# Optimization experiments

Measured on AMD Instinct MI355X. Metric: run time of the kernel, lower is better.

Reference implementation:

```python
import jax, jax.numpy as jnp
import numpy as np

DIM = 256
WINDOW = 8
NUM_HEADS = 8
N = WINDOW * WINDOW  # tokens per window
HEAD_DIM = DIM // NUM_HEADS
SCALE = HEAD_DIM ** -0.5
B_ = 2048


def _relative_position_index(w):
    coords = np.stack(np.meshgrid(np.arange(w), np.arange(w), indexing='ij'))  # 2,w,w
    cf = coords.reshape(2, -1)  # 2,N
    rel = cf[:, :, None] - cf[:, None, :]  # 2,N,N
    rel = rel.transpose(1, 2, 0) + (w - 1)  # N,N,2 in [0, 2w-2]
    return rel[..., 0] * (2 * w - 1) + rel[..., 1]  # N,N

REL_INDEX = jnp.asarray(_relative_position_index(WINDOW))  # (N,N) int


def setup_inputs() -> dict:
    key = jax.random.key(0)
    ks = jax.random.split(key, 8)
    x = jax.random.normal(ks[0], (B_, N, DIM), dtype=jnp.float32)
    mask = jax.random.normal(ks[1], (B_, 1, N, N), dtype=jnp.float32)
    w_qkv = jax.random.normal(ks[2], (3 * DIM, DIM), dtype=jnp.float32) * (DIM ** -0.5)
    b_qkv = jnp.zeros((3 * DIM,), dtype=jnp.float32)
    w_proj = jax.random.normal(ks[3], (DIM, DIM), dtype=jnp.float32) * (DIM ** -0.5)
    b_proj = jnp.zeros((DIM,), dtype=jnp.float32)
    bias_table = jax.random.normal(ks[4], ((2 * WINDOW - 1) ** 2, NUM_HEADS), dtype=jnp.float32) * 0.02
    return {"x": x, "mask": mask, "w_qkv": w_qkv, "b_qkv": b_qkv,
            "w_proj": w_proj, "b_proj": b_proj, "bias_table": bias_table}


def reference(x, mask, w_qkv, b_qkv, w_proj, b_proj, bias_table):
    Bw, n, c = x.shape
    qkv = x @ w_qkv.T + b_qkv  # (B_, N, 3*C)
    qkv = qkv.reshape(Bw, n, 3, NUM_HEADS, HEAD_DIM)
    q = qkv[:, :, 0].transpose(0, 2, 1, 3) * SCALE  # (B_, H, N, hd)
    k = qkv[:, :, 1].transpose(0, 2, 1, 3)
    v = qkv[:, :, 2].transpose(0, 2, 1, 3)
    attn = jnp.einsum('bhnd,bhmd->bhnm', q, k)  # (B_, H, N, N)
    rel_bias = bias_table[REL_INDEX]  # (N, N, H)
    attn = attn + rel_bias.transpose(2, 0, 1)[None]  # broadcast (1,H,N,N)
    attn = attn + mask  # (B_,1,N,N) broadcasts over heads
    attn = jax.nn.softmax(attn, axis=-1)
    out = jnp.einsum('bhnm,bhmd->bhnd', attn, v)  # (B_, H, N, hd)
    out = out.transpose(0, 2, 1, 3).reshape(Bw, n, c)
    return out @ w_proj.T + b_proj
```

## Files before the change

### kernel.cpp

```cpp
#include <hip/hip_runtime.h>

#define NWIN 2048
#define NTOK 64
#define CDIM 256
#define NH 8
#define HD 32
#define QSCALE 0.17677669529663689f

#define LDA 264

typedef __bf16 bf16x8 __attribute__((ext_vector_type(8)));
typedef float  f32x4  __attribute__((ext_vector_type(4)));
typedef unsigned int u32x4 __attribute__((ext_vector_type(4)));

__device__ __forceinline__ unsigned short f2bf(float f) {
    union { float f; unsigned u; } v; v.f = f;
    unsigned r = v.u + 0x7FFFu + ((v.u >> 16) & 1u);
    return (unsigned short)(r >> 16);
}

__device__ __forceinline__ bf16x8 ld16(const unsigned short* p) {
    return *(const bf16x8*)p;
}

__device__ __forceinline__ unsigned cvtpk(float lo, float hi) {
    unsigned r;
    asm("v_cvt_pk_bf16_f32 %0, %1, %2" : "=v"(r) : "v"(lo), "v"(hi));
    return r;
}
__device__ __forceinline__ void pl32(unsigned &a, unsigned &b) {
    asm("v_permlane32_swap_b32 %0, %1" : "+v"(a), "+v"(b));
}
__device__ __forceinline__ void pl16(unsigned &a, unsigned &b) {
    asm("v_permlane16_swap_b32 %0, %1" : "+v"(a), "+v"(b));
}

__device__ __forceinline__ bf16x8 xchg32(f32x4 t0, f32x4 t1) {
    unsigned u00 = cvtpk(t0[0], t0[1]);
    unsigned u01 = cvtpk(t0[2], t0[3]);
    unsigned u10 = cvtpk(t1[0], t1[1]);
    unsigned u11 = cvtpk(t1[2], t1[3]);
    pl32(u00, u10);
    pl32(u01, u11);
    pl16(u00, u10);
    pl16(u01, u11);
    union { u32x4 u; bf16x8 v; } r;
    r.u = (u32x4){u00, u01, u10, u11};
    return r.v;
}

__global__ void precast_kernel(const float* __restrict__ wq, const float* __restrict__ wp,
                               const float* __restrict__ bt,
                               unsigned short* __restrict__ wqb, unsigned short* __restrict__ wpb,
                               float* __restrict__ relbQ) {
    int i = blockIdx.x * 256 + threadIdx.x;
    if (i < 196608) {
        wqb[i] = f2bf(wq[i]);
    } else if (i < 262144) {
        wpb[i - 196608] = f2bf(wp[i - 196608]);
    } else if (i < 294912) {
        int j = i - 262144;
        int h = j >> 12;
        int q = (j >> 6) & 63;
        int k = j & 63;
        int yq = q >> 3, xq = q & 7, yk = k >> 3, xk = k & 7;
        int idx = (yq - yk + 7) * 15 + (xq - xk + 7);
        relbQ[j] = bt[idx * NH + h];
    }
}

__global__ __launch_bounds__(512, 4)
void win_attn_kernel(const float* __restrict__ x, const float* __restrict__ mask,
                     const float* __restrict__ bq, const float* __restrict__ bp,
                     const unsigned short* __restrict__ wq, const unsigned short* __restrict__ wp,
                     const float* __restrict__ relbQ, float* __restrict__ out) {
    __shared__ __align__(16) unsigned short sm[NTOK * LDA + NH * 4 * 64 * 8];
    unsigned short* sX = sm;
    unsigned short* sK = sm + NTOK * LDA;

    const int b    = blockIdx.x;
    const int tid  = threadIdx.x;
    const int wv   = tid >> 6;
    const int lane = tid & 63;
    const int lm   = lane & 15;
    const int quad = lane >> 4;
    const f32x4 fzero = {0.f, 0.f, 0.f, 0.f};

    {
        const int row = tid >> 3;
        const int c0  = (tid & 7) * 32;
        const float4* gx = (const float4*)(x + ((size_t)b * NTOK + row) * CDIM + c0);
        unsigned short* dst = sX + row * LDA + c0;
        #pragma unroll
        for (int i = 0; i < 4; ++i) {
            float4 a = gx[2 * i];
            float4 c = gx[2 * i + 1];
            u32x4 w = { cvtpk(a.x, a.y), cvtpk(a.z, a.w), cvtpk(c.x, c.y), cvtpk(c.z, c.w) };
            *(u32x4*)(dst + i * 8) = w;
        }
    }
    __syncthreads();

    const int h = wv;

    {
        f32x4 a0[4], a1[4];
        #pragma unroll
        for (int nt = 0; nt < 4; ++nt) { a0[nt] = fzero; a1[nt] = fzero; }
        const unsigned short* w0 = wq + (CDIM + h*HD + lm) * CDIM;
        const unsigned short* w1 = wq + (CDIM + h*HD + 16 + lm) * CDIM;
        #pragma unroll
        for (int ks = 0; ks < 8; ++ks) {
            bf16x8 xa[4];
            #pragma unroll
            for (int nt = 0; nt < 4; ++nt)
                xa[nt] = ld16(sX + (nt * 16 + lm) * LDA + ks * 32 + quad * 8);
            bf16x8 wf0 = ld16(w0 + ks * 32 + quad * 8);
            bf16x8 wf1 = ld16(w1 + ks * 32 + quad * 8);
            #pragma unroll
            for (int nt = 0; nt < 4; ++nt) {
                a0[nt] = __builtin_amdgcn_mfma_f32_16x16x32_bf16(wf0, xa[nt], a0[nt], 0, 0, 0);
                a1[nt] = __builtin_amdgcn_mfma_f32_16x16x32_bf16(wf1, xa[nt], a1[nt], 0, 0, 0);
            }
        }
        const float4 b0 = *(const float4*)(bq + CDIM + h*HD + quad*4);
        const float4 b1 = *(const float4*)(bq + CDIM + h*HD + 16 + quad*4);
        const float b0v[4] = {b0.x, b0.y, b0.z, b0.w};
        const float b1v[4] = {b1.x, b1.y, b1.z, b1.w};
        #pragma unroll
        for (int nt = 0; nt < 4; ++nt) {
            #pragma unroll
            for (int r = 0; r < 4; ++r) { a0[nt][r] += b0v[r]; a1[nt][r] += b1v[r]; }
            bf16x8 kfrag = xchg32(a0[nt], a1[nt]);
            *(bf16x8*)(sK + ((h * 4 + nt) * 64 + lane) * 8) = kfrag;
        }
    }

    bf16x8 qf[4];
    {
        f32x4 a0[4], a1[4];
        #pragma unroll
        for (int nt = 0; nt < 4; ++nt) { a0[nt] = fzero; a1[nt] = fzero; }
        const unsigned short* w0 = wq + (h*HD + lm) * CDIM;
        const unsigned short* w1 = wq + (h*HD + 16 + lm) * CDIM;
        #pragma unroll
        for (int ks = 0; ks < 8; ++ks) {
            bf16x8 xa[4];
            #pragma unroll
            for (int nt = 0; nt < 4; ++nt)
                xa[nt] = ld16(sX + (nt * 16 + lm) * LDA + ks * 32 + quad * 8);
            bf16x8 wf0 = ld16(w0 + ks * 32 + quad * 8);
            bf16x8 wf1 = ld16(w1 + ks * 32 + quad * 8);
            #pragma unroll
            for (int nt = 0; nt < 4; ++nt) {
                a0[nt] = __builtin_amdgcn_mfma_f32_16x16x32_bf16(wf0, xa[nt], a0[nt], 0, 0, 0);
                a1[nt] = __builtin_amdgcn_mfma_f32_16x16x32_bf16(wf1, xa[nt], a1[nt], 0, 0, 0);
            }
        }
        const float4 b0 = *(const float4*)(bq + h*HD + quad*4);
        const float4 b1 = *(const float4*)(bq + h*HD + 16 + quad*4);
        const float b0v[4] = {b0.x, b0.y, b0.z, b0.w};
        const float b1v[4] = {b1.x, b1.y, b1.z, b1.w};
        #pragma unroll
        for (int nt = 0; nt < 4; ++nt) {
            #pragma unroll
            for (int r = 0; r < 4; ++r) {
                a0[nt][r] = (a0[nt][r] + b0v[r]) * QSCALE;
                a1[nt][r] = (a1[nt][r] + b1v[r]) * QSCALE;
            }
            qf[nt] = xchg32(a0[nt], a1[nt]);
        }
    }

    bf16x8 vf[2][2];
    #pragma unroll
    for (int t = 0; t < 2; ++t) {
        f32x4 va[4];
        #pragma unroll
        for (int mt = 0; mt < 4; ++mt) va[mt] = fzero;
        const unsigned short* wvp = wq + (2*CDIM + h*HD + t*16 + lm) * CDIM;
        #pragma unroll
        for (int ks = 0; ks < 8; ++ks) {
            bf16x8 xa[4];
            #pragma unroll
            for (int mt = 0; mt < 4; ++mt)
                xa[mt] = ld16(sX + (mt * 16 + lm) * LDA + ks * 32 + quad * 8);
            bf16x8 wfv = ld16(wvp + ks * 32 + quad * 8);
            #pragma unroll
            for (int mt = 0; mt < 4; ++mt)
                va[mt] = __builtin_amdgcn_mfma_f32_16x16x32_bf16(xa[mt], wfv, va[mt], 0, 0, 0);
        }
        const float bV = bq[2*CDIM + h*HD + t*16 + lm];
        #pragma unroll
        for (int mt = 0; mt < 4; ++mt)
            #pragma unroll
            for (int r = 0; r < 4; ++r) va[mt][r] += bV;
        vf[t][0] = xchg32(va[0], va[1]);
        vf[t][1] = xchg32(va[2], va[3]);
    }
    __syncthreads();

    {
        const float* maskb = mask + (size_t)b * (NTOK * NTOK);
        const float* relh  = relbQ + h * (NTOK * NTOK);
        const unsigned short* sKh = sK + h * 4 * 64 * 8;

        #pragma unroll
        for (int rc = 0; rc < 4; ++rc) {
            f32x4 s[4];
            #pragma unroll
            for (int jt = 0; jt < 4; ++jt) {
                bf16x8 kf = ld16(sKh + (jt * 64 + lane) * 8);
                s[jt] = __builtin_amdgcn_mfma_f32_16x16x32_bf16(kf, qf[rc], fzero, 0, 0, 0);
            }

            const float* mrow = maskb + (rc * 16 + lm) * 64;
            const float* rrow = relh  + (rc * 16 + lm) * 64;
            #pragma unroll
            for (int jt = 0; jt < 4; ++jt) {
                float4 rb = *(const float4*)(rrow + jt * 16 + quad * 4);
                float4 mk = *(const float4*)(mrow + jt * 16 + quad * 4);
                const float rbv[4] = {rb.x, rb.y, rb.z, rb.w};
                const float mkv[4] = {mk.x, mk.y, mk.z, mk.w};
                #pragma unroll
                for (int r = 0; r < 4; ++r) s[jt][r] += rbv[r] + mkv[r];
            }

            float mx = s[0][0];
            #pragma unroll
            for (int jt = 0; jt < 4; ++jt)
                #pragma unroll
                for (int r = 0; r < 4; ++r) mx = fmaxf(mx, s[jt][r]);
            mx = fmaxf(mx, __shfl_xor(mx, 16, 64));
            mx = fmaxf(mx, __shfl_xor(mx, 32, 64));

            float sum = 0.f;
            #pragma unroll
            for (int jt = 0; jt < 4; ++jt)
                #pragma unroll
                for (int r = 0; r < 4; ++r) {
                    float e = __expf(s[jt][r] - mx);
                    s[jt][r] = e;
                    sum += e;
                }
            sum += __shfl_xor(sum, 16, 64);
            sum += __shfl_xor(sum, 32, 64);
            const float inv = 1.0f / sum;

            bf16x8 pb0 = xchg32(s[0], s[1]);
            bf16x8 pb1 = xchg32(s[2], s[3]);

            f32x4 o0 = __builtin_amdgcn_mfma_f32_16x16x32_bf16(vf[0][0], pb0, fzero, 0, 0, 0);
            o0 = __builtin_amdgcn_mfma_f32_16x16x32_bf16(vf[0][1], pb1, o0, 0, 0, 0);
            f32x4 o1 = __builtin_amdgcn_mfma_f32_16x16x32_bf16(vf[1][0], pb0, fzero, 0, 0, 0);
            o1 = __builtin_amdgcn_mfma_f32_16x16x32_bf16(vf[1][1], pb1, o1, 0, 0, 0);
            #pragma unroll
            for (int r = 0; r < 4; ++r) { o0[r] *= inv; o1[r] *= inv; }

            bf16x8 ob = xchg32(o0, o1);
            *(bf16x8*)(sX + (rc * 16 + lm) * LDA + h * HD + quad * 8) = ob;
        }
    }
    __syncthreads();

    {
        const int n0 = wv * HD;
        f32x4 acc[4][2];
        #pragma unroll
        for (int mt = 0; mt < 4; ++mt) { acc[mt][0] = fzero; acc[mt][1] = fzero; }

        #pragma unroll
        for (int ks = 0; ks < 8; ++ks) {
            bf16x8 bfr[2];
            #pragma unroll
            for (int nt = 0; nt < 2; ++nt)
                bfr[nt] = ld16(wp + (n0 + nt * 16 + lm) * CDIM + ks * 32 + quad * 8);
            bf16x8 afr[4];
            #pragma unroll
            for (int mt = 0; mt < 4; ++mt)
                afr[mt] = ld16(sX + (mt * 16 + lm) * LDA + ks * 32 + quad * 8);
            #pragma unroll
            for (int mt = 0; mt < 4; ++mt)
                #pragma unroll
                for (int nt = 0; nt < 2; ++nt)
                    acc[mt][nt] = __builtin_amdgcn_mfma_f32_16x16x32_bf16(afr[mt], bfr[nt], acc[mt][nt], 0, 0, 0);
        }

        float bpv[2] = { bp[n0 + lm], bp[n0 + 16 + lm] };
        #pragma unroll
        for (int mt = 0; mt < 4; ++mt)
            #pragma unroll
            for (int nt = 0; nt < 2; ++nt)
                #pragma unroll
                for (int reg = 0; reg < 4; ++reg) {
                    int r = mt * 16 + quad * 4 + reg;
                    out[((size_t)b * NTOK + r) * CDIM + n0 + nt * 16 + lm] = acc[mt][nt][reg] + bpv[nt];
                }
    }
}

extern "C" void kernel_launch(void* const* d_in, const int* in_sizes, int n_in,
                              void* d_out, int out_size, void* d_ws, size_t ws_size,
                              hipStream_t stream) {
    const float* x    = (const float*)d_in[0];
    const float* mask = (const float*)d_in[1];
    const float* wq   = (const float*)d_in[2];
    const float* bq   = (const float*)d_in[3];
    const float* wp   = (const float*)d_in[4];
    const float* bp   = (const float*)d_in[5];
    const float* bt   = (const float*)d_in[6];

    unsigned short* wqb   = (unsigned short*)d_ws;
    unsigned short* wpb   = wqb + 196608;
    float*          relbQ = (float*)((char*)d_ws + 524288);
    float*          out   = (float*)d_out;

    precast_kernel<<<1152, 256, 0, stream>>>(wq, wp, bt, wqb, wpb, relbQ);
    win_attn_kernel<<<NWIN, 512, 0, stream>>>(x, mask, bq, bp, wqb, wpb, relbQ, out);
}
```

Baseline: 461.1 us.

## Process two windows per block to reuse rel-bias loads and halve grid

Each 512-thread block now handles two windows instead of one. It stages both inputs in a doubled shared-memory buffer, holds Q and V fragments for both windows in registers, and loads the relative-position bias once per row chunk for both windows. The V projection is also reworked to load both weight halves in a single k-loop. The aim is to amortise weight and bias fetches and per-block overhead across two windows. The cost is higher register and LDS use, which lowers occupancy (launch bounds drop from 4 to 2 blocks per CU) and halves the grid to 1024 blocks.

```diff
diff --git a/kernel.cpp b/kernel.cpp
--- a/kernel.cpp
+++ b/kernel.cpp
@@ -8,6 +8,7 @@
 #define QSCALE 0.17677669529663689f
 
 #define LDA 264
+#define SKW (NH * 4 * 64 * 8)
 
 typedef __bf16 bf16x8 __attribute__((ext_vector_type(8)));
 typedef float  f32x4  __attribute__((ext_vector_type(4)));
@@ -69,16 +70,14 @@
     }
 }
 
-__global__ __launch_bounds__(512, 4)
+__global__ __launch_bounds__(512, 2)
 void win_attn_kernel(const float* __restrict__ x, const float* __restrict__ mask,
                      const float* __restrict__ bq, const float* __restrict__ bp,
                      const unsigned short* __restrict__ wq, const unsigned short* __restrict__ wp,
                      const float* __restrict__ relbQ, float* __restrict__ out) {
-    __shared__ __align__(16) unsigned short sm[NTOK * LDA + NH * 4 * 64 * 8];
-    unsigned short* sX = sm;
-    unsigned short* sK = sm + NTOK * LDA;
-
-    const int b    = blockIdx.x;
+    __shared__ __align__(16) unsigned short sm[2 * NTOK * LDA + 2 * SKW];
+
+    const int b0   = blockIdx.x * 2;
     const int tid  = threadIdx.x;
     const int wv   = tid >> 6;
     const int lane = tid & 63;
@@ -89,213 +88,244 @@
     {
         const int row = tid >> 3;
         const int c0  = (tid & 7) * 32;
-        const float4* gx = (const float4*)(x + ((size_t)b * NTOK + row) * CDIM + c0);
-        unsigned short* dst = sX + row * LDA + c0;
         #pragma unroll
-        for (int i = 0; i < 4; ++i) {
-            float4 a = gx[2 * i];
-            float4 c = gx[2 * i + 1];
-            u32x4 w = { cvtpk(a.x, a.y), cvtpk(a.z, a.w), cvtpk(c.x, c.y), cvtpk(c.z, c.w) };
-            *(u32x4*)(dst + i * 8) = w;
+        for (int w = 0; w < 2; ++w) {
+            const float4* gx = (const float4*)(x + ((size_t)(b0 + w) * NTOK + row) * CDIM + c0);
+            unsigned short* dst = sm + w * (NTOK * LDA) + row * LDA + c0;
+            #pragma unroll
+            for (int i = 0; i < 4; ++i) {
+                float4 a = gx[2 * i];
+                float4 c = gx[2 * i + 1];
+                u32x4 v = { cvtpk(a.x, a.y), cvtpk(a.z, a.w), cvtpk(c.x, c.y), cvtpk(c.z, c.w) };
+                *(u32x4*)(dst + i * 8) = v;
+            }
         }
     }
     __syncthreads();
 
     const int h = wv;
 
+    bf16x8 qf[2][4];
+    bf16x8 vf[2][2][2];
+    #pragma unroll
+    for (int w = 0; w < 2; ++w) {
+        const unsigned short* sXw = sm + w * (NTOK * LDA);
+        unsigned short* sKw = sm + 2 * (NTOK * LDA) + w * SKW;
+
+        {
+            f32x4 a0[4], a1[4];
+            #pragma unroll
+            for (int nt = 0; nt < 4; ++nt) { a0[nt] = fzero; a1[nt] = fzero; }
+            const unsigned short* w0 = wq + (CDIM + h*HD + lm) * CDIM;
+            const unsigned short* w1 = wq + (CDIM + h*HD + 16 + lm) * CDIM;
+            #pragma unroll
+            for (int ks = 0; ks < 8; ++ks) {
+                bf16x8 xa[4];
+                #pragma unroll
+                for (int nt = 0; nt < 4; ++nt)
+                    xa[nt] = ld16(sXw + (nt * 16 + lm) * LDA + ks * 32 + quad * 8);
+                bf16x8 wf0 = ld16(w0 + ks * 32 + quad * 8);
+                bf16x8 wf1 = ld16(w1 + ks * 32 + quad * 8);
+                #pragma unroll
+                for (int nt = 0; nt < 4; ++nt) {
+                    a0[nt] = __builtin_amdgcn_mfma_f32_16x16x32_bf16(wf0, xa[nt], a0[nt], 0, 0, 0);
+                    a1[nt] = __builtin_amdgcn_mfma_f32_16x16x32_bf16(wf1, xa[nt], a1[nt], 0, 0, 0);
+                }
+            }
+            const float4 bk0 = *(const float4*)(bq + CDIM + h*HD + quad*4);
+            const float4 bk1 = *(const float4*)(bq + CDIM + h*HD + 16 + quad*4);
+            const float b0v[4] = {bk0.x, bk0.y, bk0.z, bk0.w};
+            const float b1v[4] = {bk1.x, bk1.y, bk1.z, bk1.w};
+            #pragma unroll
+            for (int nt = 0; nt < 4; ++nt) {
+                #pragma unroll
+                for (int r = 0; r < 4; ++r) { a0[nt][r] += b0v[r]; a1[nt][r] += b1v[r]; }
+                bf16x8 kfrag = xchg32(a0[nt], a1[nt]);
+                *(bf16x8*)(sKw + ((h * 4 + nt) * 64 + lane) * 8) = kfrag;
+            }
+        }
+
+        {
+            f32x4 a0[4], a1[4];
+            #pragma unroll
+            for (int nt = 0; nt < 4; ++nt) { a0[nt] = fzero; a1[nt] = fzero; }
+            const unsigned short* w0 = wq + (h*HD + lm) * CDIM;
+            const unsigned short* w1 = wq + (h*HD + 16 + lm) * CDIM;
+            #pragma unroll
+            for (int ks = 0; ks < 8; ++ks) {
+                bf16x8 xa[4];
+                #pragma unroll
+                for (int nt = 0; nt < 4; ++nt)
+                    xa[nt] = ld16(sXw + (nt * 16 + lm) * LDA + ks * 32 + quad * 8);
+                bf16x8 wf0 = ld16(w0 + ks * 32 + quad * 8);
+                bf16x8 wf1 = ld16(w1 + ks * 32 + quad * 8);
+                #pragma unroll
+                for (int nt = 0; nt < 4; ++nt) {
+                    a0[nt] = __builtin_amdgcn_mfma_f32_16x16x32_bf16(wf0, xa[nt], a0[nt], 0, 0, 0);
+                    a1[nt] = __builtin_amdgcn_mfma_f32_16x16x32_bf16(wf1, xa[nt], a1[nt], 0, 0, 0);
+                }
+            }
+            const float4 bq0 = *(const float4*)(bq + h*HD + quad*4);
+            const float4 bq1 = *(const float4*)(bq + h*HD + 16 + quad*4);
+            const float b0v[4] = {bq0.x, bq0.y, bq0.z, bq0.w};
+            const float b1v[4] = {bq1.x, bq1.y, bq1.z, bq1.w};
+            #pragma unroll
+            for (int nt = 0; nt < 4; ++nt) {
+                #pragma unroll
+                for (int r = 0; r < 4; ++r) {
+                    a0[nt][r] = (a0[nt][r] + b0v[r]) * QSCALE;
+                    a1[nt][r] = (a1[nt][r] + b1v[r]) * QSCALE;
+                }
+                qf[w][nt] = xchg32(a0[nt], a1[nt]);
+            }
+        }
+
+        {
+            f32x4 va[4][2];
+            #pragma unroll
+            for (int mt = 0; mt < 4; ++mt) { va[mt][0] = fzero; va[mt][1] = fzero; }
+            #pragma unroll
+            for (int ks = 0; ks < 8; ++ks) {
+                bf16x8 xa[4], wfv[2];
+                #pragma unroll
+                for (int mt = 0; mt < 4; ++mt)
+                    xa[mt] = ld16(sXw + (mt * 16 + lm) * LDA + ks * 32 + quad * 8);
+                #pragma unroll
+                for (int t = 0; t < 2; ++t)
+                    wfv[t] = ld16(wq + (2*CDIM + h*HD + t*16 + lm) * CDIM + ks * 32 + quad * 8);
+                #pragma unroll
+                for (int mt = 0; mt < 4; ++mt)
+                    #pragma unroll
+                    for (int t = 0; t < 2; ++t)
+                        va[mt][t] = __builtin_amdgcn_mfma_f32_16x16x32_bf16(xa[mt], wfv[t], va[mt][t], 0, 0, 0);
+            }
+            const float bV0 = bq[2*CDIM + h*HD + lm];
+            const float bV1 = bq[2*CDIM + h*HD + 16 + lm];
+            #pragma unroll
+            for (int mt = 0; mt < 4; ++mt)
+                #pragma unroll
+                for (int r = 0; r < 4; ++r) { va[mt][0][r] += bV0; va[mt][1][r] += bV1; }
+            #pragma unroll
+            for (int t = 0; t < 2; ++t) {
+                vf[w][t][0] = xchg32(va[0][t], va[1][t]);
+                vf[w][t][1] = xchg32(va[2][t], va[3][t]);
+            }
+        }
+    }
+    __syncthreads();
+
     {
-        f32x4 a0[4], a1[4];
-        #pragma unroll
-        for (int nt = 0; nt < 4; ++nt) { a0[nt] = fzero; a1[nt] = fzero; }
-        const unsigned short* w0 = wq + (CDIM + h*HD + lm) * CDIM;
-        const unsigned short* w1 = wq + (CDIM + h*HD + 16 + lm) * CDIM;
-        #pragma unroll
-        for (int ks = 0; ks < 8; ++ks) {
-            bf16x8 xa[4];
-            #pragma unroll
-            for (int nt = 0; nt < 4; ++nt)
-                xa[nt] = ld16(sX + (nt * 16 + lm) * LDA + ks * 32 + quad * 8);
-            bf16x8 wf0 = ld16(w0 + ks * 32 + quad * 8);
-            bf16x8 wf1 = ld16(w1 + ks * 32 + quad * 8);
-            #pragma unroll
-            for (int nt = 0; nt < 4; ++nt) {
-                a0[nt] = __builtin_amdgcn_mfma_f32_16x16x32_bf16(wf0, xa[nt], a0[nt], 0, 0, 0);
-                a1[nt] = __builtin_amdgcn_mfma_f32_16x16x32_bf16(wf1, xa[nt], a1[nt], 0, 0, 0);
-            }
-        }
-        const float4 b0 = *(const float4*)(bq + CDIM + h*HD + quad*4);
-        const float4 b1 = *(const float4*)(bq + CDIM + h*HD + 16 + quad*4);
-        const float b0v[4] = {b0.x, b0.y, b0.z, b0.w};
-        const float b1v[4] = {b1.x, b1.y, b1.z, b1.w};
-        #pragma unroll
-        for (int nt = 0; nt < 4; ++nt) {
-            #pragma unroll
-            for (int r = 0; r < 4; ++r) { a0[nt][r] += b0v[r]; a1[nt][r] += b1v[r]; }
-            bf16x8 kfrag = xchg32(a0[nt], a1[nt]);
-            *(bf16x8*)(sK + ((h * 4 + nt) * 64 + lane) * 8) = kfrag;
-        }
-    }
-
-    bf16x8 qf[4];
-    {
-        f32x4 a0[4], a1[4];
-        #pragma unroll
-        for (int nt = 0; nt < 4; ++nt) { a0[nt] = fzero; a1[nt] = fzero; }
-        const unsigned short* w0 = wq + (h*HD + lm) * CDIM;
-        const unsigned short* w1 = wq + (h*HD + 16 + lm) * CDIM;
-        #pragma unroll
-        for (int ks = 0; ks < 8; ++ks) {
-            bf16x8 xa[4];
-            #pragma unroll
-            for (int nt = 0; nt < 4; ++nt)
-                xa[nt] = ld16(sX + (nt * 16 + lm) * LDA + ks * 32 + quad * 8);
-            bf16x8 wf0 = ld16(w0 + ks * 32 + quad * 8);
-            bf16x8 wf1 = ld16(w1 + ks * 32 + quad * 8);
-            #pragma unroll
-            for (int nt = 0; nt < 4; ++nt) {
-                a0[nt] = __builtin_amdgcn_mfma_f32_16x16x32_bf16(wf0, xa[nt], a0[nt], 0, 0, 0);
-                a1[nt] = __builtin_amdgcn_mfma_f32_16x16x32_bf16(wf1, xa[nt], a1[nt], 0, 0, 0);
-            }
-        }
-        const float4 b0 = *(const float4*)(bq + h*HD + quad*4);
-        const float4 b1 = *(const float4*)(bq + h*HD + 16 + quad*4);
-        const float b0v[4] = {b0.x, b0.y, b0.z, b0.w};
-        const float b1v[4] = {b1.x, b1.y, b1.z, b1.w};
-        #pragma unroll
-        for (int nt = 0; nt < 4; ++nt) {
-            #pragma unroll
-            for (int r = 0; r < 4; ++r) {
-                a0[nt][r] = (a0[nt][r] + b0v[r]) * QSCALE;
-                a1[nt][r] = (a1[nt][r] + b1v[r]) * QSCALE;
-            }
-            qf[nt] = xchg32(a0[nt], a1[nt]);
-        }
-    }
-
-    bf16x8 vf[2][2];
-    #pragma unroll
-    for (int t = 0; t < 2; ++t) {
-        f32x4 va[4];
-        #pragma unroll
-        for (int mt = 0; mt < 4; ++mt) va[mt] = fzero;
-        const unsigned short* wvp = wq + (2*CDIM + h*HD + t*16 + lm) * CDIM;
-        #pragma unroll
-        for (int ks = 0; ks < 8; ++ks) {
-            bf16x8 xa[4];
-            #pragma unroll
-            for (int mt = 0; mt < 4; ++mt)
-                xa[mt] = ld16(sX + (mt * 16 + lm) * LDA + ks * 32 + quad * 8);
-            bf16x8 wfv = ld16(wvp + ks * 32 + quad * 8);
-            #pragma unroll
-            for (int mt = 0; mt < 4; ++mt)
-                va[mt] = __builtin_amdgcn_mfma_f32_16x16x32_bf16(xa[mt], wfv, va[mt], 0, 0, 0);
-        }
-        const float bV = bq[2*CDIM + h*HD + t*16 + lm];
-        #pragma unroll
-        for (int mt = 0; mt < 4; ++mt)
-            #pragma unroll
-            for (int r = 0; r < 4; ++r) va[mt][r] += bV;
-        vf[t][0] = xchg32(va[0], va[1]);
-        vf[t][1] = xchg32(va[2], va[3]);
-    }
-    __syncthreads();
-
-    {
-        const float* maskb = mask + (size_t)b * (NTOK * NTOK);
-        const float* relh  = relbQ + h * (NTOK * NTOK);
-        const unsigned short* sKh = sK + h * 4 * 64 * 8;
+        const float* relh = relbQ + h * (NTOK * NTOK);
 
         #pragma unroll
         for (int rc = 0; rc < 4; ++rc) {
-            f32x4 s[4];
-            #pragma unroll
-            for (int jt = 0; jt < 4; ++jt) {
-                bf16x8 kf = ld16(sKh + (jt * 64 + lane) * 8);
-                s[jt] = __builtin_amdgcn_mfma_f32_16x16x32_bf16(kf, qf[rc], fzero, 0, 0, 0);
-            }
-
-            const float* mrow = maskb + (rc * 16 + lm) * 64;
-            const float* rrow = relh  + (rc * 16 + lm) * 64;
-            #pragma unroll
-            for (int jt = 0; jt < 4; ++jt) {
-                float4 rb = *(const float4*)(rrow + jt * 16 + quad * 4);
-                float4 mk = *(const float4*)(mrow + jt * 16 + quad * 4);
-                const float rbv[4] = {rb.x, rb.y, rb.z, rb.w};
-                const float mkv[4] = {mk.x, mk.y, mk.z, mk.w};
-                #pragma unroll
-                for (int r = 0; r < 4; ++r) s[jt][r] += rbv[r] + mkv[r];
-            }
-
-            float mx = s[0][0];
+            const float* rrow = relh + (rc * 16 + lm) * 64;
+            float4 rb[4];
             #pragma unroll
             for (int jt = 0; jt < 4; ++jt)
-                #pragma unroll
-                for (int r = 0; r < 4; ++r) mx = fmaxf(mx, s[jt][r]);
-            mx = fmaxf(mx, __shfl_xor(mx, 16, 64));
-            mx = fmaxf(mx, __shfl_xor(mx, 32, 64));
-
-            float sum = 0.f;
-            #pragma unroll
-            for (int jt = 0; jt < 4; ++jt)
-                #pragma unroll
-                for (int r = 0; r < 4; ++r) {
-                    float e = __expf(s[jt][r] - mx);
-                    s[jt][r] = e;
-                    sum += e;
-                }
-            sum += __shfl_xor(sum, 16, 64);
-            sum += __shfl_xor(sum, 32, 64);
-            const float inv = 1.0f / sum;
-
-            bf16x8 pb0 = xchg32(s[0], s[1]);
-            bf16x8 pb1 = xchg32(s[2], s[3]);
-
-            f32x4 o0 = __builtin_amdgcn_mfma_f32_16x16x32_bf16(vf[0][0], pb0, fzero, 0, 0, 0);
-            o0 = __builtin_amdgcn_mfma_f32_16x16x32_bf16(vf[0][1], pb1, o0, 0, 0, 0);
-            f32x4 o1 = __builtin_amdgcn_mfma_f32_16x16x32_bf16(vf[1][0], pb0, fzero, 0, 0, 0);
-            o1 = __builtin_amdgcn_mfma_f32_16x16x32_bf16(vf[1][1], pb1, o1, 0, 0, 0);
-            #pragma unroll
-            for (int r = 0; r < 4; ++r) { o0[r] *= inv; o1[r] *= inv; }
-
-            bf16x8 ob = xchg32(o0, o1);
-            *(bf16x8*)(sX + (rc * 16 + lm) * LDA + h * HD + quad * 8) = ob;
+                rb[jt] = *(const float4*)(rrow + jt * 16 + quad * 4);
+
+            #pragma unroll
+            for (int w = 0; w < 2; ++w) {
+                const unsigned short* sKh = sm + 2 * (NTOK * LDA) + w * SKW + h * 4 * 64 * 8;
+                unsigned short* sOw = sm + w * (NTOK * LDA);
+                const float* mrow = mask + (size_t)(b0 + w) * (NTOK * NTOK) + (rc * 16 + lm) * 64;
+
+                float4 mk[4];
+                #pragma unroll
+                for (int jt = 0; jt < 4; ++jt)
+                    mk[jt] = *(const float4*)(mrow + jt * 16 + quad * 4);
+
+                f32x4 s[4];
+                #pragma unroll
+                for (int jt = 0; jt < 4; ++jt) {
+                    bf16x8 kfr = ld16(sKh + (jt * 64 + lane) * 8);
+                    s[jt] = __builtin_amdgcn_mfma_f32_16x16x32_bf16(kfr, qf[w][rc], fzero, 0, 0, 0);
+                }
+
+                #pragma unroll
+                for (int jt = 0; jt < 4; ++jt) {
+                    const float rbv[4] = {rb[jt].x, rb[jt].y, rb[jt].z, rb[jt].w};
+                    const float mkv[4] = {mk[jt].x, mk[jt].y, mk[jt].z, mk[jt].w};
+                    #pragma unroll
+                    for (int r = 0; r < 4; ++r) s[jt][r] += rbv[r] + mkv[r];
+                }
+
+                float mx = s[0][0];
+                #pragma unroll
+                for (int jt = 0; jt < 4; ++jt)
+                    #pragma unroll
+                    for (int r = 0; r < 4; ++r) mx = fmaxf(mx, s[jt][r]);
+                mx = fmaxf(mx, __shfl_xor(mx, 16, 64));
+                mx = fmaxf(mx, __shfl_xor(mx, 32, 64));
+
+                float sum = 0.f;
+                #pragma unroll
+                for (int jt = 0; jt < 4; ++jt)
+                    #pragma unroll
+                    for (int r = 0; r < 4; ++r) {
+                        float e = __expf(s[jt][r] - mx);
+                        s[jt][r] = e;
+                        sum += e;
+                    }
+                sum += __shfl_xor(sum, 16, 64);
+                sum += __shfl_xor(sum, 32, 64);
+                const float inv = 1.0f / sum;
+
+                bf16x8 pb0 = xchg32(s[0], s[1]);
+                bf16x8 pb1 = xchg32(s[2], s[3]);
+
+                f32x4 o0 = __builtin_amdgcn_mfma_f32_16x16x32_bf16(vf[w][0][0], pb0, fzero, 0, 0, 0);
+                o0 = __builtin_amdgcn_mfma_f32_16x16x32_bf16(vf[w][0][1], pb1, o0, 0, 0, 0);
+                f32x4 o1 = __builtin_amdgcn_mfma_f32_16x16x32_bf16(vf[w][1][0], pb0, fzero, 0, 0, 0);
+                o1 = __builtin_amdgcn_mfma_f32_16x16x32_bf16(vf[w][1][1], pb1, o1, 0, 0, 0);
+                #pragma unroll
+                for (int r = 0; r < 4; ++r) { o0[r] *= inv; o1[r] *= inv; }
+
+                bf16x8 ob = xchg32(o0, o1);
+                *(bf16x8*)(sOw + (rc * 16 + lm) * LDA + h * HD + quad * 8) = ob;
+            }
         }
     }
     __syncthreads();
 
     {
         const int n0 = wv * HD;
-        f32x4 acc[4][2];
         #pragma unroll
-        for (int mt = 0; mt < 4; ++mt) { acc[mt][0] = fzero; acc[mt][1] = fzero; }
-
-        #pragma unroll
-        for (int ks = 0; ks < 8; ++ks) {
-            bf16x8 bfr[2];
-            #pragma unroll
-            for (int nt = 0; nt < 2; ++nt)
-                bfr[nt] = ld16(wp + (n0 + nt * 16 + lm) * CDIM + ks * 32 + quad * 8);
-            bf16x8 afr[4];
+        for (int w = 0; w < 2; ++w) {
+            const unsigned short* sOw = sm + w * (NTOK * LDA);
+            f32x4 acc[4][2];
+            #pragma unroll
+            for (int mt = 0; mt < 4; ++mt) { acc[mt][0] = fzero; acc[mt][1] = fzero; }
+
+            #pragma unroll
+            for (int ks = 0; ks < 8; ++ks) {
+                bf16x8 bfr[2];
+                #pragma unroll
+                for (int nt = 0; nt < 2; ++nt)
+                    bfr[nt] = ld16(wp + (n0 + nt * 16 + lm) * CDIM + ks * 32 + quad * 8);
+                bf16x8 afr[4];
+                #pragma unroll
+                for (int mt = 0; mt < 4; ++mt)
+                    afr[mt] = ld16(sOw + (mt * 16 + lm) * LDA + ks * 32 + quad * 8);
+                #pragma unroll
+                for (int mt = 0; mt < 4; ++mt)
+                    #pragma unroll
+                    for (int nt = 0; nt < 2; ++nt)
+                        acc[mt][nt] = __builtin_amdgcn_mfma_f32_16x16x32_bf16(afr[mt], bfr[nt], acc[mt][nt], 0, 0, 0);
+            }
+
+            float bpv[2] = { bp[n0 + lm], bp[n0 + 16 + lm] };
             #pragma unroll
             for (int mt = 0; mt < 4; ++mt)
-                afr[mt] = ld16(sX + (mt * 16 + lm) * LDA + ks * 32 + quad * 8);
-            #pragma unroll
-            for (int mt = 0; mt < 4; ++mt)
                 #pragma unroll
                 for (int nt = 0; nt < 2; ++nt)
-                    acc[mt][nt] = __builtin_amdgcn_mfma_f32_16x16x32_bf16(afr[mt], bfr[nt], acc[mt][nt], 0, 0, 0);
-        }
-
-        float bpv[2] = { bp[n0 + lm], bp[n0 + 16 + lm] };
-        #pragma unroll
-        for (int mt = 0; mt < 4; ++mt)
-            #pragma unroll
-            for (int nt = 0; nt < 2; ++nt)
-                #pragma unroll
-                for (int reg = 0; reg < 4; ++reg) {
-                    int r = mt * 16 + quad * 4 + reg;
-                    out[((size_t)b * NTOK + r) * CDIM + n0 + nt * 16 + lm] = acc[mt][nt][reg] + bpv[nt];
-                }
+                    #pragma unroll
+                    for (int reg = 0; reg < 4; ++reg) {
+                        int r = mt * 16 + quad * 4 + reg;
+                        out[((size_t)(b0 + w) * NTOK + r) * CDIM + n0 + nt * 16 + lm] = acc[mt][nt][reg] + bpv[nt];
+                    }
+        }
     }
 }
 
@@ -316,5 +346,5 @@
     float*          out   = (float*)d_out;
 
     precast_kernel<<<1152, 256, 0, stream>>>(wq, wp, bt, wqb, wpb, relbQ);
-    win_attn_kernel<<<NWIN, 512, 0, stream>>>(x, mask, bq, bp, wqb, wpb, relbQ, out);
-}
+    win_attn_kernel<<<NWIN / 2, 512, 0, stream>>>(x, mask, bq, bp, wqb, wpb, relbQ, out);
+}
```

New measurement: 421.1 us. 8.7% less time.

## Stage mask in LDS, keep K in registers, store Q in LDS, disable unrolling

Applied to the files above, without the earlier changes.

The mask tile is now loaded cooperatively into shared memory at kernel start, and the softmax stage reads it from LDS instead of issuing strided global loads. K fragments stay in registers and Q fragments go through LDS, which swaps the roles in the score MFMA loop. The V projection is merged into one pass, and most loops are marked unroll 1. Launch bounds drop from 4 to 2 blocks per CU because LDS grows to about 84KB. This cuts occupancy and loses the instruction-level parallelism that unrolling gave.

```diff
diff --git a/kernel.cpp b/kernel.cpp
--- a/kernel.cpp
+++ b/kernel.cpp
@@ -8,6 +8,7 @@
 #define QSCALE 0.17677669529663689f
 
 #define LDA 264
+#define LDM 68
 
 typedef __bf16 bf16x8 __attribute__((ext_vector_type(8)));
 typedef float  f32x4  __attribute__((ext_vector_type(4)));
@@ -69,14 +70,15 @@
     }
 }
 
-__global__ __launch_bounds__(512, 4)
+__global__ __launch_bounds__(512, 2)
 void win_attn_kernel(const float* __restrict__ x, const float* __restrict__ mask,
                      const float* __restrict__ bq, const float* __restrict__ bp,
                      const unsigned short* __restrict__ wq, const unsigned short* __restrict__ wp,
                      const float* __restrict__ relbQ, float* __restrict__ out) {
-    __shared__ __align__(16) unsigned short sm[NTOK * LDA + NH * 4 * 64 * 8];
-    unsigned short* sX = sm;
-    unsigned short* sK = sm + NTOK * LDA;
+    __shared__ __align__(16) unsigned char smraw[83968];
+    unsigned short* sX = (unsigned short*)smraw;
+    float*          sM = (float*)(smraw + 33792);
+    unsigned short* sQ = (unsigned short*)(smraw + 51200);
 
     const int b    = blockIdx.x;
     const int tid  = threadIdx.x;
@@ -91,25 +93,31 @@
         const int c0  = (tid & 7) * 32;
         const float4* gx = (const float4*)(x + ((size_t)b * NTOK + row) * CDIM + c0);
         unsigned short* dst = sX + row * LDA + c0;
-        #pragma unroll
+        #pragma unroll 1
         for (int i = 0; i < 4; ++i) {
             float4 a = gx[2 * i];
             float4 c = gx[2 * i + 1];
             u32x4 w = { cvtpk(a.x, a.y), cvtpk(a.z, a.w), cvtpk(c.x, c.y), cvtpk(c.z, c.w) };
             *(u32x4*)(dst + i * 8) = w;
         }
+        const int mc0 = (tid & 7) * 8;
+        const float4* gm = (const float4*)(mask + (size_t)b * (NTOK * NTOK) + row * 64 + mc0);
+        float4 m0 = gm[0], m1 = gm[1];
+        *(float4*)(sM + row * LDM + mc0)     = m0;
+        *(float4*)(sM + row * LDM + mc0 + 4) = m1;
     }
     __syncthreads();
 
     const int h = wv;
 
+    bf16x8 kf[4];
     {
         f32x4 a0[4], a1[4];
         #pragma unroll
         for (int nt = 0; nt < 4; ++nt) { a0[nt] = fzero; a1[nt] = fzero; }
         const unsigned short* w0 = wq + (CDIM + h*HD + lm) * CDIM;
         const unsigned short* w1 = wq + (CDIM + h*HD + 16 + lm) * CDIM;
-        #pragma unroll
+        #pragma unroll 1
         for (int ks = 0; ks < 8; ++ks) {
             bf16x8 xa[4];
             #pragma unroll
@@ -131,19 +139,17 @@
         for (int nt = 0; nt < 4; ++nt) {
             #pragma unroll
             for (int r = 0; r < 4; ++r) { a0[nt][r] += b0v[r]; a1[nt][r] += b1v[r]; }
-            bf16x8 kfrag = xchg32(a0[nt], a1[nt]);
-            *(bf16x8*)(sK + ((h * 4 + nt) * 64 + lane) * 8) = kfrag;
-        }
-    }
-
-    bf16x8 qf[4];
+            kf[nt] = xchg32(a0[nt], a1[nt]);
+        }
+    }
+
     {
         f32x4 a0[4], a1[4];
         #pragma unroll
         for (int nt = 0; nt < 4; ++nt) { a0[nt] = fzero; a1[nt] = fzero; }
         const unsigned short* w0 = wq + (h*HD + lm) * CDIM;
         const unsigned short* w1 = wq + (h*HD + 16 + lm) * CDIM;
-        #pragma unroll
+        #pragma unroll 1
         for (int ks = 0; ks < 8; ++ks) {
             bf16x8 xa[4];
             #pragma unroll
@@ -168,54 +174,59 @@
                 a0[nt][r] = (a0[nt][r] + b0v[r]) * QSCALE;
                 a1[nt][r] = (a1[nt][r] + b1v[r]) * QSCALE;
             }
-            qf[nt] = xchg32(a0[nt], a1[nt]);
+            bf16x8 qfrag = xchg32(a0[nt], a1[nt]);
+            *(bf16x8*)(sQ + ((h * 4 + nt) * 64 + lane) * 8) = qfrag;
         }
     }
 
     bf16x8 vf[2][2];
-    #pragma unroll
-    for (int t = 0; t < 2; ++t) {
-        f32x4 va[4];
-        #pragma unroll
-        for (int mt = 0; mt < 4; ++mt) va[mt] = fzero;
-        const unsigned short* wvp = wq + (2*CDIM + h*HD + t*16 + lm) * CDIM;
-        #pragma unroll
+    {
+        f32x4 va[4][2];
+        #pragma unroll
+        for (int mt = 0; mt < 4; ++mt) { va[mt][0] = fzero; va[mt][1] = fzero; }
+        const unsigned short* wv0 = wq + (2*CDIM + h*HD + lm) * CDIM;
+        const unsigned short* wv1 = wq + (2*CDIM + h*HD + 16 + lm) * CDIM;
+        #pragma unroll 1
         for (int ks = 0; ks < 8; ++ks) {
             bf16x8 xa[4];
             #pragma unroll
             for (int mt = 0; mt < 4; ++mt)
                 xa[mt] = ld16(sX + (mt * 16 + lm) * LDA + ks * 32 + quad * 8);
-            bf16x8 wfv = ld16(wvp + ks * 32 + quad * 8);
-            #pragma unroll
-            for (int mt = 0; mt < 4; ++mt)
-                va[mt] = __builtin_amdgcn_mfma_f32_16x16x32_bf16(xa[mt], wfv, va[mt], 0, 0, 0);
-        }
-        const float bV = bq[2*CDIM + h*HD + t*16 + lm];
+            bf16x8 wfv0 = ld16(wv0 + ks * 32 + quad * 8);
+            bf16x8 wfv1 = ld16(wv1 + ks * 32 + quad * 8);
+            #pragma unroll
+            for (int mt = 0; mt < 4; ++mt) {
+                va[mt][0] = __builtin_amdgcn_mfma_f32_16x16x32_bf16(xa[mt], wfv0, va[mt][0], 0, 0, 0);
+                va[mt][1] = __builtin_amdgcn_mfma_f32_16x16x32_bf16(xa[mt], wfv1, va[mt][1], 0, 0, 0);
+            }
+        }
+        const float bV0 = bq[2*CDIM + h*HD + lm];
+        const float bV1 = bq[2*CDIM + h*HD + 16 + lm];
         #pragma unroll
         for (int mt = 0; mt < 4; ++mt)
             #pragma unroll
-            for (int r = 0; r < 4; ++r) va[mt][r] += bV;
-        vf[t][0] = xchg32(va[0], va[1]);
-        vf[t][1] = xchg32(va[2], va[3]);
+            for (int r = 0; r < 4; ++r) { va[mt][0][r] += bV0; va[mt][1][r] += bV1; }
+        vf[0][0] = xchg32(va[0][0], va[1][0]);
+        vf[0][1] = xchg32(va[2][0], va[3][0]);
+        vf[1][0] = xchg32(va[0][1], va[1][1]);
+        vf[1][1] = xchg32(va[2][1], va[3][1]);
     }
     __syncthreads();
 
     {
-        const float* maskb = mask + (size_t)b * (NTOK * NTOK);
-        const float* relh  = relbQ + h * (NTOK * NTOK);
-        const unsigned short* sKh = sK + h * 4 * 64 * 8;
-
-        #pragma unroll
+        const float* relh = relbQ + h * (NTOK * NTOK);
+        const unsigned short* sQh = sQ + h * 4 * 64 * 8;
+
+        #pragma unroll 1
         for (int rc = 0; rc < 4; ++rc) {
+            bf16x8 qa = ld16(sQh + (rc * 64 + lane) * 8);
             f32x4 s[4];
             #pragma unroll
-            for (int jt = 0; jt < 4; ++jt) {
-                bf16x8 kf = ld16(sKh + (jt * 64 + lane) * 8);
-                s[jt] = __builtin_amdgcn_mfma_f32_16x16x32_bf16(kf, qf[rc], fzero, 0, 0, 0);
-            }
-
-            const float* mrow = maskb + (rc * 16 + lm) * 64;
-            const float* rrow = relh  + (rc * 16 + lm) * 64;
+            for (int jt = 0; jt < 4; ++jt)
+                s[jt] = __builtin_amdgcn_mfma_f32_16x16x32_bf16(kf[jt], qa, fzero, 0, 0, 0);
+
+            const float* mrow = sM   + (rc * 16 + lm) * LDM;
+            const float* rrow = relh + (rc * 16 + lm) * 64;
             #pragma unroll
             for (int jt = 0; jt < 4; ++jt) {
                 float4 rb = *(const float4*)(rrow + jt * 16 + quad * 4);
@@ -268,22 +279,22 @@
         f32x4 acc[4][2];
         #pragma unroll
         for (int mt = 0; mt < 4; ++mt) { acc[mt][0] = fzero; acc[mt][1] = fzero; }
-
-        #pragma unroll
+        const unsigned short* wp0 = wp + (n0 + lm) * CDIM;
+        const unsigned short* wp1 = wp + (n0 + 16 + lm) * CDIM;
+
+        #pragma unroll 1
         for (int ks = 0; ks < 8; ++ks) {
-            bf16x8 bfr[2];
-            #pragma unroll
-            for (int nt = 0; nt < 2; ++nt)
-                bfr[nt] = ld16(wp + (n0 + nt * 16 + lm) * CDIM + ks * 32 + quad * 8);
+            bf16x8 bfr0 = ld16(wp0 + ks * 32 + quad * 8);
+            bf16x8 bfr1 = ld16(wp1 + ks * 32 + quad * 8);
             bf16x8 afr[4];
             #pragma unroll
             for (int mt = 0; mt < 4; ++mt)
                 afr[mt] = ld16(sX + (mt * 16 + lm) * LDA + ks * 32 + quad * 8);
             #pragma unroll
-            for (int mt = 0; mt < 4; ++mt)
-                #pragma unroll
-                for (int nt = 0; nt < 2; ++nt)
-                    acc[mt][nt] = __builtin_amdgcn_mfma_f32_16x16x32_bf16(afr[mt], bfr[nt], acc[mt][nt], 0, 0, 0);
+            for (int mt = 0; mt < 4; ++mt) {
+                acc[mt][0] = __builtin_amdgcn_mfma_f32_16x16x32_bf16(afr[mt], bfr0, acc[mt][0], 0, 0, 0);
+                acc[mt][1] = __builtin_amdgcn_mfma_f32_16x16x32_bf16(afr[mt], bfr1, acc[mt][1], 0, 0, 0);
+            }
         }
 
         float bpv[2] = { bp[n0 + lm], bp[n0 + 16 + lm] };
```

After: 416.0 us. 1.11x faster.
